# Performance work log

Hardware: AMD Instinct MI355X
Metric: run time of the kernel (lower is better)

Reference implementation:

```python
import jax, jax.numpy as jnp
import numpy as np

EMBED = 1024
HEADS = 16
HEAD_DIM = EMBED // HEADS
DIVIDER = int(np.sqrt(HEAD_DIM))  # torch code uses int(sqrt(head_dim)) == 8


def setup_inputs() -> dict:
    key = jax.random.key(0)
    ks = jax.random.split(key, 9)
    B, S = 2, 2048
    scale = 1.0 / np.sqrt(EMBED)
    def lin(kw, kb):
        W = jax.random.uniform(kw, (EMBED, EMBED), jnp.float32, -scale, scale)
        b = jax.random.uniform(kb, (EMBED,), jnp.float32, -scale, scale)
        return W, b
    Wq, bq = lin(ks[0], ks[1])
    Wk, bk = lin(ks[2], ks[3])
    Wv, bv = lin(ks[4], ks[5])
    Wo, bo = lin(ks[6], ks[7])
    x = jax.random.normal(ks[8], (B, S, EMBED), jnp.float32)
    return {"x": x, "Wq": Wq, "bq": bq, "Wk": Wk, "bk": bk,
            "Wv": Wv, "bv": bv, "Wo": Wo, "bo": bo}


def reference(x, Wq, bq, Wk, bk, Wv, bv, Wo, bo):
    B, S, _ = x.shape
    # projections (torch Linear: x @ W.T + b)
    q = x @ Wq.T + bq
    k = x @ Wk.T + bk
    v = x @ Wv.T + bv
    # split heads: [B, S, H, D] -> [B, H, S, D]
    def heads(t):
        return t.reshape(B, S, HEADS, HEAD_DIM).transpose(0, 2, 1, 3)
    q, k, v = heads(q), heads(k), heads(v)
    # scores [B, H, S, S]
    scores = jnp.einsum('bhsd,bhtd->bhst', q, k) / DIVIDER
    attn = jax.nn.softmax(scores, axis=-1)
    out = jnp.einsum('bhst,bhtd->bhsd', attn, v)
    out = out.transpose(0, 2, 1, 3).reshape(B, S, EMBED)
    return out @ Wo.T + bo
```

## Files before the change

kernel.cpp:

```cpp
#include <hip/hip_runtime.h>
#include <hip/hip_bf16.h>
#include <stdint.h>

using bf16 = __hip_bfloat16;
typedef __attribute__((ext_vector_type(8))) short   short8;
typedef __attribute__((ext_vector_type(4))) float   floatx4;

static __device__ __forceinline__ unsigned short f2bf(float f) {
    return __builtin_bit_cast(unsigned short, __float2bfloat16(f));
}

static __device__ __forceinline__ uint4 load8bf(const void* p, size_t e, int f) {
    if (!f) return *(const uint4*)((const ushort*)p + e);
    const float* fp = (const float*)p + e;
    float4 a = *(const float4*)fp;
    float4 b = *(const float4*)(fp + 4);
    union { uint4 u; unsigned short s[8]; } r;
    r.s[0] = f2bf(a.x); r.s[1] = f2bf(a.y); r.s[2] = f2bf(a.z); r.s[3] = f2bf(a.w);
    r.s[4] = f2bf(b.x); r.s[5] = f2bf(b.y); r.s[6] = f2bf(b.z); r.s[7] = f2bf(b.w);
    return r.u;
}
static __device__ __forceinline__ float loadScalar(const void* p, int i, int f) {
    return f ? ((const float*)p)[i] : __bfloat162float(((const bf16*)p)[i]);
}

__global__ void detect_dtype(const ushort* __restrict__ x, int* __restrict__ flag) {
    __shared__ int cnt;
    if (threadIdx.x == 0) cnt = 0;
    __syncthreads();
    unsigned short u = x[threadIdx.x * 2];
    int e = (u >> 7) & 0xFF;
    int bad = (e > 133 || e < 94) ? 1 : 0;
    atomicAdd(&cnt, bad);
    __syncthreads();
    if (threadIdx.x == 0) *flag = (cnt > 64) ? 1 : 0;
}

__global__ __launch_bounds__(512, 4)
void gemm_bt(const void* __restrict__ A,
             const void* __restrict__ Wa, const void* __restrict__ Wb,
             const void* __restrict__ Ba, const void* __restrict__ Bb,
             void* __restrict__ Oa, void* __restrict__ Ob_,
             int pa, int pb, int a_ext, int out_ext,
             const int* __restrict__ flagp)
{
    __shared__ ushort pool[12288];

    const int f  = *flagp;
    const int fA = a_ext ? f : 0;
    const int z  = blockIdx.z;
    const void* W   = z ? Wb : Wa;
    const void* Bi  = z ? Bb : Ba;
    void*       Out = z ? Ob_ : Oa;
    const int   pm  = z ? pb : pa;

    const int m0 = blockIdx.x * 128;
    const int n0 = blockIdx.y * 64;
    const int tid  = threadIdx.x;
    const int lane = tid & 63;
    const int wave = tid >> 6;
    const int r15  = lane & 15;
    const int quad = lane >> 4;

    const int srow = tid >> 3;
    const int sg   = tid & 7;

    ushort* xs  = pool;
    ushort* wsm = pool + 8192;

    floatx4 acc[4];
#pragma unroll
    for (int db = 0; db < 4; db++) acc[db] = (floatx4){0.f, 0.f, 0.f, 0.f};

    uint4 apre[2], wpre;
#pragma unroll
    for (int p = 0; p < 2; p++)
        apre[p] = load8bf(A, (size_t)(m0 + srow + p * 64) * 1024 + sg * 8, fA);
    wpre = load8bf(W, (size_t)(n0 + srow) * 1024 + sg * 8, f);

    for (int kb = 0; kb < 1024; kb += 64) {
#pragma unroll
        for (int p = 0; p < 2; p++) {
            int row = srow + p * 64;
            *(uint4*)(&xs[row * 64 + ((sg ^ (row & 7)) << 3)]) = apre[p];
        }
        *(uint4*)(&wsm[srow * 64 + ((sg ^ (srow & 7)) << 3)]) = wpre;
        __syncthreads();
        if (kb + 64 < 1024) {
#pragma unroll
            for (int p = 0; p < 2; p++)
                apre[p] = load8bf(A, (size_t)(m0 + srow + p * 64) * 1024
                                      + kb + 64 + sg * 8, fA);
            wpre = load8bf(W, (size_t)(n0 + srow) * 1024 + kb + 64 + sg * 8, f);
        }
#pragma unroll
        for (int ks = 0; ks < 2; ks++) {
            int arow = wave * 16 + r15;
            short8 af = *(const short8*)(
                &xs[arow * 64 + (((ks * 4 + quad) ^ (arow & 7)) << 3)]);
#pragma unroll
            for (int db = 0; db < 4; db++) {
                int brow = db * 16 + r15;
                short8 bv = *(const short8*)(
                    &wsm[brow * 64 + (((ks * 4 + quad) ^ (brow & 7)) << 3)]);
                acc[db] = __builtin_amdgcn_mfma_f32_16x16x32_bf16(
                    af, bv, acc[db], 0, 0, 0);
            }
        }
        __syncthreads();
    }

    if (pm == 2) {
#pragma unroll
        for (int db = 0; db < 4; db++) {
            int d = db * 16 + r15;
            float bias = loadScalar(Bi, n0 + d, f);
            int s4 = wave * 16 + quad * 4;
            union { uint2 u; ushort us[4]; } pk;
#pragma unroll
            for (int r = 0; r < 4; r++) pk.us[r] = f2bf(acc[db][r] + bias);
            *(uint2*)(&pool[d * 128 + (((s4 >> 3) ^ (d & 15)) << 3) + (s4 & 7)])
                = pk.u;
        }
        __syncthreads();
        const int b_  = m0 >> 11;
        const int h   = n0 >> 6;
        const int sl0 = m0 & 2047;
#pragma unroll
        for (int rr = 0; rr < 2; rr++) {
            int idx = rr * 512 + tid;
            int d = idx >> 4, sgrp = idx & 15;
            uint4 v = *(const uint4*)(&pool[d * 128 + ((sgrp ^ (d & 15)) << 3)]);
            *(uint4*)((ushort*)Out +
                      ((size_t)((b_ * 16 + h) * 64 + d) << 11) + sl0 + sgrp * 8) = v;
        }
        return;
    }

#pragma unroll
    for (int db = 0; db < 4; db++) {
        int col = n0 + db * 16 + r15;
        float bias = loadScalar(Bi, col, f);
#pragma unroll
        for (int r = 0; r < 4; r++) {
            int row = m0 + wave * 16 + quad * 4 + r;
            float v = acc[db][r] + bias;
            if (pm == 1) {
                int h = col >> 6, d = col & 63;
                int b_ = row >> 11, s = row & 2047;
                ((ushort*)Out)[(((size_t)(b_ * 16 + h) * 2048 + s) << 6) + d]
                    = f2bf(v);
            } else if (out_ext && f) {
                ((float*)Out)[(size_t)row * 1024 + col] = v;
            } else {
                ((ushort*)Out)[(size_t)row * 1024 + col] = f2bf(v);
            }
        }
    }
}

__global__ __launch_bounds__(512, 4)
void attn_fused(const void* __restrict__ x, const void* __restrict__ Wq,
                const void* __restrict__ bq,
                const ushort* __restrict__ K, const ushort* __restrict__ VT,
                ushort* __restrict__ AO, const int* __restrict__ flagp)
{
    __shared__ ushort pool[24576];

    const int f   = *flagp;
    const int bh  = blockIdx.x;
    const int h   = bh & 15, b_ = bh >> 4;
    const int q0  = blockIdx.y * 128;
    const int tid  = threadIdx.x;
    const int lane = tid & 63;
    const int wave = tid >> 6;
    const int r15  = lane & 15;
    const int quad = lane >> 4;
    const size_t base = (size_t)bh << 17;

    const int srow = tid >> 3;
    const int sg   = tid & 7;

    uint4 kpre = *(const uint4*)(K  + base + (size_t)srow * 64   + sg * 8);
    uint4 vpre = *(const uint4*)(VT + base + (size_t)srow * 2048 + sg * 8);

    floatx4 qacc[4];
#pragma unroll
    for (int db = 0; db < 4; db++) qacc[db] = (floatx4){0.f,0.f,0.f,0.f};

    uint4 xpre[2], wpre;
#pragma unroll
    for (int p = 0; p < 2; p++)
        xpre[p] = load8bf(x, (size_t)(b_ * 2048 + q0 + srow + p * 64) * 1024
                              + sg * 8, f);
    wpre = load8bf(Wq, (size_t)(h * 64 + srow) * 1024 + sg * 8, f);

    for (int kb = 0; kb < 1024; kb += 64) {
        int buf = (kb >> 6) & 1;
        ushort* xs  = pool + buf * 8192;
        ushort* wsm = pool + 16384 + buf * 4096;
#pragma unroll
        for (int p = 0; p < 2; p++) {
            int row = srow + p * 64;
            *(uint4*)(&xs[row * 64 + ((sg ^ (row & 7)) << 3)]) = xpre[p];
        }
        *(uint4*)(&wsm[srow * 64 + ((sg ^ (srow & 7)) << 3)]) = wpre;
        __syncthreads();
        if (kb + 64 < 1024) {
#pragma unroll
            for (int p = 0; p < 2; p++)
                xpre[p] = load8bf(x, (size_t)(b_ * 2048 + q0 + srow + p * 64) * 1024
                                      + kb + 64 + sg * 8, f);
            wpre = load8bf(Wq, (size_t)(h * 64 + srow) * 1024 + kb + 64 + sg * 8, f);
        }
#pragma unroll
        for (int ks = 0; ks < 2; ks++) {
            int arow = wave * 16 + r15;
            short8 af = *(const short8*)(
                &xs[arow * 64 + (((ks * 4 + quad) ^ (arow & 7)) << 3)]);
#pragma unroll
            for (int db = 0; db < 4; db++) {
                int brow = db * 16 + r15;
                short8 bv = *(const short8*)(
                    &wsm[brow * 64 + (((ks * 4 + quad) ^ (brow & 7)) << 3)]);
                qacc[db] = __builtin_amdgcn_mfma_f32_16x16x32_bf16(
                    af, bv, qacc[db], 0, 0, 0);
            }
        }
    }

    ushort* Qs = pool;
    const float csc = 0.1803368801f;
#pragma unroll
    for (int db = 0; db < 4; db++) {
        int d = db * 16 + r15;
        float bias = loadScalar(bq, h * 64 + d, f);
#pragma unroll
        for (int r = 0; r < 4; r++) {
            int q = wave * 16 + quad * 4 + r;
            Qs[q * 64 + (((d >> 3) ^ (q & 7)) << 3) + (d & 7)] =
                f2bf((qacc[db][r] + bias) * csc);
        }
    }
    short8 qf[2];
#pragma unroll
    for (int ks = 0; ks < 2; ks++) {
        int arow = wave * 16 + r15;
        qf[ks] = *(const short8*)(
            &Qs[arow * 64 + (((ks * 4 + quad) ^ (arow & 7)) << 3)]);
    }
    __syncthreads();

    floatx4 oacc[4], lacc;
#pragma unroll
    for (int db = 0; db < 4; db++) oacc[db] = (floatx4){0.f,0.f,0.f,0.f};
    lacc = (floatx4){0.f,0.f,0.f,0.f};
    short8 ones;
#pragma unroll
    for (int j = 0; j < 8; j++) ones[j] = (short)0x3F80;
    ushort* Ps = pool + 16384;
    const int e7 = (r15 & 7) << 1;

    for (int t0 = 0; t0 < 2048; t0 += 64) {
        int buf = (t0 >> 6) & 1;
        ushort* Ks = pool + buf * 4096;
        ushort* Vt = pool + 8192 + buf * 4096;
        *(uint4*)(&Ks[srow * 64 + ((sg ^ (srow & 7)) << 3)]) = kpre;
        *(uint4*)(&Vt[srow * 64 + ((sg ^ (srow & 7)) << 3)]) = vpre;
        __syncthreads();
        if (t0 < 1984) {
            kpre = *(const uint4*)(K  + base + (size_t)(t0 + 64 + srow) * 64
                                       + sg * 8);
            vpre = *(const uint4*)(VT + base + (size_t)srow * 2048
                                       + t0 + 64 + sg * 8);
        }

        floatx4 s[4];
#pragma unroll
        for (int mb = 0; mb < 4; mb++) s[mb] = (floatx4){0.f,0.f,0.f,0.f};
#pragma unroll
        for (int ks = 0; ks < 2; ks++)
#pragma unroll
            for (int mb = 0; mb < 4; mb++) {
                int arow = mb * 16 + r15;
                short8 kf = *(const short8*)(
                    &Ks[arow * 64 + (((ks * 4 + quad) ^ (arow & 7)) << 3)]);
                s[mb] = __builtin_amdgcn_mfma_f32_16x16x32_bf16(
                    kf, qf[ks], s[mb], 0, 0, 0);
            }

#pragma unroll
        for (int mb = 0; mb < 4; mb++) {
            int q  = wave * 16 + r15;
            int tg = (mb * 4 + quad) ^ e7;
            uint b0 = __builtin_bit_cast(uint, __builtin_amdgcn_exp2f(s[mb][0]));
            uint b1 = __builtin_bit_cast(uint, __builtin_amdgcn_exp2f(s[mb][1]));
            uint b2 = __builtin_bit_cast(uint, __builtin_amdgcn_exp2f(s[mb][2]));
            uint b3 = __builtin_bit_cast(uint, __builtin_amdgcn_exp2f(s[mb][3]));
            uint2 pk;
            pk.x = (b1 & 0xFFFF0000u) | (b0 >> 16);
            pk.y = (b3 & 0xFFFF0000u) | (b2 >> 16);
            *(uint2*)(&Ps[q * 64 + tg * 4]) = pk;
        }

#pragma unroll
        for (int ks2 = 0; ks2 < 2; ks2++) {
            int q   = wave * 16 + r15;
            int tg0 = (ks2 * 8 + quad * 2) ^ e7;
            short8 pf = *(const short8*)(&Ps[q * 64 + tg0 * 4]);
#pragma unroll
            for (int db = 0; db < 4; db++) {
                int brow = db * 16 + r15;
                short8 vf = *(const short8*)(
                    &Vt[brow * 64 + (((ks2 * 4 + quad) ^ (brow & 7)) << 3)]);
                oacc[db] = __builtin_amdgcn_mfma_f32_16x16x32_bf16(
                    pf, vf, oacc[db], 0, 0, 0);
            }
            lacc = __builtin_amdgcn_mfma_f32_16x16x32_bf16(
                pf, ones, lacc, 0, 0, 0);
        }
    }

    float inv[4];
#pragma unroll
    for (int r = 0; r < 4; r++) inv[r] = 1.f / lacc[r];
#pragma unroll
    for (int db = 0; db < 4; db++) {
        int d = db * 16 + r15;
#pragma unroll
        for (int r = 0; r < 4; r++) {
            int qi = q0 + wave * 16 + quad * 4 + r;
            AO[((size_t)(b_ * 2048 + qi) << 10) + h * 64 + d] =
                f2bf(oacc[db][r] * inv[r]);
        }
    }
}

__global__ void copy_u4(const uint4* __restrict__ src, uint4* __restrict__ dst) {
    size_t i = (size_t)blockIdx.x * 256 + threadIdx.x;
    dst[i] = src[i];
}

extern "C" void kernel_launch(void* const* d_in, const int* in_sizes, int n_in,
                              void* d_out, int out_size, void* d_ws, size_t ws_size,
                              hipStream_t stream)
{
    const void* x  = d_in[0];
    const void* Wq = d_in[1];
    const void* bq = d_in[2];
    const void* Wk = d_in[3];
    const void* bk = d_in[4];
    const void* Wv = d_in[5];
    const void* bv = d_in[6];
    const void* Wo = d_in[7];
    const void* bo = d_in[8];

    const size_t TEN = (size_t)2 * 16 * 2048 * 64;
    int*    flagp = (int*)d_ws;
    ushort* Kw    = (ushort*)((char*)d_ws + 256);
    ushort* Vw    = Kw + TEN;
    const bool big_ws = ws_size >= 3 * TEN * sizeof(ushort) + 256;
    ushort* AOw   = big_ws ? (Vw + TEN) : (ushort*)d_out;
    ushort* Oin   = big_ws ? AOw : Kw;

    detect_dtype<<<1, 256, 0, stream>>>((const ushort*)x, flagp);

    gemm_bt<<<dim3(32, 16, 2), dim3(512), 0, stream>>>(
        x, Wk, Wv, bk, bv, Kw, Vw, 1, 2, 1,
        0, flagp);

    attn_fused<<<dim3(32, 16), dim3(512), 0, stream>>>(
        x, Wq, bq, Kw, Vw, AOw, flagp);

    if (!big_ws)
        copy_u4<<<dim3(2048), dim3(256), 0, stream>>>(
            (const uint4*)d_out, (uint4*)Oin);

    gemm_bt<<<dim3(32, 16, 1), dim3(512), 0, stream>>>(
        Oin, Wo, Wo, bo, bo, d_out, d_out, 0, 0, 0,
        1, flagp);
}
```

Measured before the change: 226.2 us.

## Halve attention block threads, give each wave two 16-row query tiles

The fused attention kernel now runs 4 waves of 256 threads instead of 8, and each wave handles 32 query rows as two 16-row sub-tiles. K and V fragments read from shared memory are reused across both sub-tiles, which halves LDS reads per MFMA in the Q projection, QK^T and PV stages. Staging loads are doubled per thread to cover the same tile. In exchange it raises register pressure (doubled accumulators), lowers per-block parallelism, and changes launch bounds to 256 threads with 3 blocks per CU, which may reduce occupancy.

```diff
diff --git a/kernel.cpp b/kernel.cpp
--- a/kernel.cpp
+++ b/kernel.cpp
@@ -159,7 +159,7 @@
     }
 }
 
-__global__ __launch_bounds__(512, 4)
+__global__ __launch_bounds__(256, 3)
 void attn_fused(const void* __restrict__ x, const void* __restrict__ Wq,
                 const void* __restrict__ bq,
                 const ushort* __restrict__ K, const ushort* __restrict__ VT,
@@ -181,50 +181,73 @@
     const int srow = tid >> 3;
     const int sg   = tid & 7;
 
-    uint4 kpre = *(const uint4*)(K  + base + (size_t)srow * 64   + sg * 8);
-    uint4 vpre = *(const uint4*)(VT + base + (size_t)srow * 2048 + sg * 8);
-
-    floatx4 qacc[4];
-#pragma unroll
-    for (int db = 0; db < 4; db++) qacc[db] = (floatx4){0.f,0.f,0.f,0.f};
-
-    uint4 xpre[2], wpre;
+    uint4 kpre[2], vpre[2];
+#pragma unroll
+    for (int p = 0; p < 2; p++) {
+        kpre[p] = *(const uint4*)(K  + base + (size_t)(srow + p * 32) * 64
+                                      + sg * 8);
+        vpre[p] = *(const uint4*)(VT + base + (size_t)(srow + p * 32) * 2048
+                                      + sg * 8);
+    }
+
+    floatx4 qacc[2][4];
+#pragma unroll
+    for (int qb = 0; qb < 2; qb++)
+#pragma unroll
+        for (int db = 0; db < 4; db++) qacc[qb][db] = (floatx4){0.f,0.f,0.f,0.f};
+
+    uint4 xpre[4], wpre[2];
+#pragma unroll
+    for (int p = 0; p < 4; p++)
+        xpre[p] = load8bf(x, (size_t)(b_ * 2048 + q0 + srow + p * 32) * 1024
+                              + sg * 8, f);
 #pragma unroll
     for (int p = 0; p < 2; p++)
-        xpre[p] = load8bf(x, (size_t)(b_ * 2048 + q0 + srow + p * 64) * 1024
-                              + sg * 8, f);
-    wpre = load8bf(Wq, (size_t)(h * 64 + srow) * 1024 + sg * 8, f);
+        wpre[p] = load8bf(Wq, (size_t)(h * 64 + srow + p * 32) * 1024 + sg * 8, f);
 
     for (int kb = 0; kb < 1024; kb += 64) {
         int buf = (kb >> 6) & 1;
         ushort* xs  = pool + buf * 8192;
         ushort* wsm = pool + 16384 + buf * 4096;
 #pragma unroll
+        for (int p = 0; p < 4; p++) {
+            int row = srow + p * 32;
+            *(uint4*)(&xs[row * 64 + ((sg ^ (row & 7)) << 3)]) = xpre[p];
+        }
+#pragma unroll
         for (int p = 0; p < 2; p++) {
-            int row = srow + p * 64;
-            *(uint4*)(&xs[row * 64 + ((sg ^ (row & 7)) << 3)]) = xpre[p];
-        }
-        *(uint4*)(&wsm[srow * 64 + ((sg ^ (srow & 7)) << 3)]) = wpre;
+            int row = srow + p * 32;
+            *(uint4*)(&wsm[row * 64 + ((sg ^ (row & 7)) << 3)]) = wpre[p];
+        }
         __syncthreads();
         if (kb + 64 < 1024) {
 #pragma unroll
+            for (int p = 0; p < 4; p++)
+                xpre[p] = load8bf(x, (size_t)(b_ * 2048 + q0 + srow + p * 32) * 1024
+                                      + kb + 64 + sg * 8, f);
+#pragma unroll
             for (int p = 0; p < 2; p++)
-                xpre[p] = load8bf(x, (size_t)(b_ * 2048 + q0 + srow + p * 64) * 1024
+                wpre[p] = load8bf(Wq, (size_t)(h * 64 + srow + p * 32) * 1024
                                       + kb + 64 + sg * 8, f);
-            wpre = load8bf(Wq, (size_t)(h * 64 + srow) * 1024 + kb + 64 + sg * 8, f);
         }
 #pragma unroll
         for (int ks = 0; ks < 2; ks++) {
-            int arow = wave * 16 + r15;
-            short8 af = *(const short8*)(
-                &xs[arow * 64 + (((ks * 4 + quad) ^ (arow & 7)) << 3)]);
+            short8 af[2];
+#pragma unroll
+            for (int qb = 0; qb < 2; qb++) {
+                int arow = wave * 32 + qb * 16 + r15;
+                af[qb] = *(const short8*)(
+                    &xs[arow * 64 + (((ks * 4 + quad) ^ (arow & 7)) << 3)]);
+            }
 #pragma unroll
             for (int db = 0; db < 4; db++) {
                 int brow = db * 16 + r15;
                 short8 bv = *(const short8*)(
                     &wsm[brow * 64 + (((ks * 4 + quad) ^ (brow & 7)) << 3)]);
-                qacc[db] = __builtin_amdgcn_mfma_f32_16x16x32_bf16(
-                    af, bv, qacc[db], 0, 0, 0);
+#pragma unroll
+                for (int qb = 0; qb < 2; qb++)
+                    qacc[qb][db] = __builtin_amdgcn_mfma_f32_16x16x32_bf16(
+                        af[qb], bv, qacc[qb][db], 0, 0, 0);
             }
         }
     }
@@ -232,29 +255,36 @@
     ushort* Qs = pool;
     const float csc = 0.1803368801f;
 #pragma unroll
-    for (int db = 0; db < 4; db++) {
-        int d = db * 16 + r15;
-        float bias = loadScalar(bq, h * 64 + d, f);
-#pragma unroll
-        for (int r = 0; r < 4; r++) {
-            int q = wave * 16 + quad * 4 + r;
-            Qs[q * 64 + (((d >> 3) ^ (q & 7)) << 3) + (d & 7)] =
-                f2bf((qacc[db][r] + bias) * csc);
-        }
-    }
-    short8 qf[2];
-#pragma unroll
-    for (int ks = 0; ks < 2; ks++) {
-        int arow = wave * 16 + r15;
-        qf[ks] = *(const short8*)(
-            &Qs[arow * 64 + (((ks * 4 + quad) ^ (arow & 7)) << 3)]);
-    }
+    for (int qb = 0; qb < 2; qb++)
+#pragma unroll
+        for (int db = 0; db < 4; db++) {
+            int d = db * 16 + r15;
+            float bias = loadScalar(bq, h * 64 + d, f);
+#pragma unroll
+            for (int r = 0; r < 4; r++) {
+                int q = wave * 32 + qb * 16 + quad * 4 + r;
+                Qs[q * 64 + (((d >> 3) ^ (q & 7)) << 3) + (d & 7)] =
+                    f2bf((qacc[qb][db][r] + bias) * csc);
+            }
+        }
+    short8 qf[2][2];
+#pragma unroll
+    for (int qb = 0; qb < 2; qb++)
+#pragma unroll
+        for (int ks = 0; ks < 2; ks++) {
+            int arow = wave * 32 + qb * 16 + r15;
+            qf[qb][ks] = *(const short8*)(
+                &Qs[arow * 64 + (((ks * 4 + quad) ^ (arow & 7)) << 3)]);
+        }
     __syncthreads();
 
-    floatx4 oacc[4], lacc;
-#pragma unroll
-    for (int db = 0; db < 4; db++) oacc[db] = (floatx4){0.f,0.f,0.f,0.f};
-    lacc = (floatx4){0.f,0.f,0.f,0.f};
+    floatx4 oacc[2][4], lacc[2];
+#pragma unroll
+    for (int qb = 0; qb < 2; qb++) {
+#pragma unroll
+        for (int db = 0; db < 4; db++) oacc[qb][db] = (floatx4){0.f,0.f,0.f,0.f};
+        lacc[qb] = (floatx4){0.f,0.f,0.f,0.f};
+    }
     short8 ones;
 #pragma unroll
     for (int j = 0; j < 8; j++) ones[j] = (short)0x3F80;
@@ -265,19 +295,28 @@
         int buf = (t0 >> 6) & 1;
         ushort* Ks = pool + buf * 4096;
         ushort* Vt = pool + 8192 + buf * 4096;
-        *(uint4*)(&Ks[srow * 64 + ((sg ^ (srow & 7)) << 3)]) = kpre;
-        *(uint4*)(&Vt[srow * 64 + ((sg ^ (srow & 7)) << 3)]) = vpre;
+#pragma unroll
+        for (int p = 0; p < 2; p++) {
+            int row = srow + p * 32;
+            *(uint4*)(&Ks[row * 64 + ((sg ^ (row & 7)) << 3)]) = kpre[p];
+            *(uint4*)(&Vt[row * 64 + ((sg ^ (row & 7)) << 3)]) = vpre[p];
+        }
         __syncthreads();
         if (t0 < 1984) {
-            kpre = *(const uint4*)(K  + base + (size_t)(t0 + 64 + srow) * 64
-                                       + sg * 8);
-            vpre = *(const uint4*)(VT + base + (size_t)srow * 2048
-                                       + t0 + 64 + sg * 8);
-        }
-
-        floatx4 s[4];
-#pragma unroll
-        for (int mb = 0; mb < 4; mb++) s[mb] = (floatx4){0.f,0.f,0.f,0.f};
+#pragma unroll
+            for (int p = 0; p < 2; p++) {
+                kpre[p] = *(const uint4*)(K  + base
+                              + (size_t)(t0 + 64 + srow + p * 32) * 64 + sg * 8);
+                vpre[p] = *(const uint4*)(VT + base
+                              + (size_t)(srow + p * 32) * 2048 + t0 + 64 + sg * 8);
+            }
+        }
+
+        floatx4 s[4][2];
+#pragma unroll
+        for (int mb = 0; mb < 4; mb++)
+#pragma unroll
+            for (int qb = 0; qb < 2; qb++) s[mb][qb] = (floatx4){0.f,0.f,0.f,0.f};
 #pragma unroll
         for (int ks = 0; ks < 2; ks++)
 #pragma unroll
@@ -285,55 +324,72 @@
                 int arow = mb * 16 + r15;
                 short8 kf = *(const short8*)(
                     &Ks[arow * 64 + (((ks * 4 + quad) ^ (arow & 7)) << 3)]);
-                s[mb] = __builtin_amdgcn_mfma_f32_16x16x32_bf16(
-                    kf, qf[ks], s[mb], 0, 0, 0);
-            }
-
-#pragma unroll
-        for (int mb = 0; mb < 4; mb++) {
-            int q  = wave * 16 + r15;
-            int tg = (mb * 4 + quad) ^ e7;
-            uint b0 = __builtin_bit_cast(uint, __builtin_amdgcn_exp2f(s[mb][0]));
-            uint b1 = __builtin_bit_cast(uint, __builtin_amdgcn_exp2f(s[mb][1]));
-            uint b2 = __builtin_bit_cast(uint, __builtin_amdgcn_exp2f(s[mb][2]));
-            uint b3 = __builtin_bit_cast(uint, __builtin_amdgcn_exp2f(s[mb][3]));
-            uint2 pk;
-            pk.x = (b1 & 0xFFFF0000u) | (b0 >> 16);
-            pk.y = (b3 & 0xFFFF0000u) | (b2 >> 16);
-            *(uint2*)(&Ps[q * 64 + tg * 4]) = pk;
+#pragma unroll
+                for (int qb = 0; qb < 2; qb++)
+                    s[mb][qb] = __builtin_amdgcn_mfma_f32_16x16x32_bf16(
+                        kf, qf[qb][ks], s[mb][qb], 0, 0, 0);
+            }
+
+#pragma unroll
+        for (int qb = 0; qb < 2; qb++) {
+            int q = wave * 32 + qb * 16 + r15;
+#pragma unroll
+            for (int mb = 0; mb < 4; mb++) {
+                int tg = (mb * 4 + quad) ^ e7;
+                uint b0 = __builtin_bit_cast(uint, __builtin_amdgcn_exp2f(s[mb][qb][0]));
+                uint b1 = __builtin_bit_cast(uint, __builtin_amdgcn_exp2f(s[mb][qb][1]));
+                uint b2 = __builtin_bit_cast(uint, __builtin_amdgcn_exp2f(s[mb][qb][2]));
+                uint b3 = __builtin_bit_cast(uint, __builtin_amdgcn_exp2f(s[mb][qb][3]));
+                uint2 pk;
+                pk.x = (b1 & 0xFFFF0000u) | (b0 >> 16);
+                pk.y = (b3 & 0xFFFF0000u) | (b2 >> 16);
+                *(uint2*)(&Ps[q * 64 + tg * 4]) = pk;
+            }
         }
 
 #pragma unroll
         for (int ks2 = 0; ks2 < 2; ks2++) {
-            int q   = wave * 16 + r15;
-            int tg0 = (ks2 * 8 + quad * 2) ^ e7;
-            short8 pf = *(const short8*)(&Ps[q * 64 + tg0 * 4]);
+            short8 pf[2];
+#pragma unroll
+            for (int qb = 0; qb < 2; qb++) {
+                int q   = wave * 32 + qb * 16 + r15;
+                int tg0 = (ks2 * 8 + quad * 2) ^ e7;
+                pf[qb] = *(const short8*)(&Ps[q * 64 + tg0 * 4]);
+            }
 #pragma unroll
             for (int db = 0; db < 4; db++) {
                 int brow = db * 16 + r15;
                 short8 vf = *(const short8*)(
                     &Vt[brow * 64 + (((ks2 * 4 + quad) ^ (brow & 7)) << 3)]);
-                oacc[db] = __builtin_amdgcn_mfma_f32_16x16x32_bf16(
-                    pf, vf, oacc[db], 0, 0, 0);
-            }
-            lacc = __builtin_amdgcn_mfma_f32_16x16x32_bf16(
-                pf, ones, lacc, 0, 0, 0);
-        }
-    }
-
-    float inv[4];
-#pragma unroll
-    for (int r = 0; r < 4; r++) inv[r] = 1.f / lacc[r];
-#pragma unroll
-    for (int db = 0; db < 4; db++) {
-        int d = db * 16 + r15;
-#pragma unroll
-        for (int r = 0; r < 4; r++) {
-            int qi = q0 + wave * 16 + quad * 4 + r;
-            AO[((size_t)(b_ * 2048 + qi) << 10) + h * 64 + d] =
-                f2bf(oacc[db][r] * inv[r]);
-        }
-    }
+#pragma unroll
+                for (int qb = 0; qb < 2; qb++)
+                    oacc[qb][db] = __builtin_amdgcn_mfma_f32_16x16x32_bf16(
+                        pf[qb], vf, oacc[qb][db], 0, 0, 0);
+            }
+#pragma unroll
+            for (int qb = 0; qb < 2; qb++)
+                lacc[qb] = __builtin_amdgcn_mfma_f32_16x16x32_bf16(
+                    pf[qb], ones, lacc[qb], 0, 0, 0);
+        }
+    }
+
+    float inv[2][4];
+#pragma unroll
+    for (int qb = 0; qb < 2; qb++)
+#pragma unroll
+        for (int r = 0; r < 4; r++) inv[qb][r] = 1.f / lacc[qb][r];
+#pragma unroll
+    for (int qb = 0; qb < 2; qb++)
+#pragma unroll
+        for (int db = 0; db < 4; db++) {
+            int d = db * 16 + r15;
+#pragma unroll
+            for (int r = 0; r < 4; r++) {
+                int qi = q0 + wave * 32 + qb * 16 + quad * 4 + r;
+                AO[((size_t)(b_ * 2048 + qi) << 10) + h * 64 + d] =
+                    f2bf(oacc[qb][db][r] * inv[qb][r]);
+            }
+        }
 }
 
 __global__ void copy_u4(const uint4* __restrict__ src, uint4* __restrict__ dst) {
@@ -369,7 +425,7 @@
         x, Wk, Wv, bk, bv, Kw, Vw, 1, 2, 1,
         0, flagp);
 
-    attn_fused<<<dim3(32, 16), dim3(512), 0, stream>>>(
+    attn_fused<<<dim3(32, 16), dim3(256), 0, stream>>>(
         x, Wq, bq, Kw, Vw, AOw, flagp);
 
     if (!big_ws)
```

Measured after the change: 274.7 us. +21.4%, slower.
